# Kernel tuning notes

Hardware: AMD Instinct MI355X
Metric: run time of the kernel (lower is better)

## Reference

```python
import jax, jax.numpy as jnp
import numpy as np

N = 10000   # nodes
E = 320000  # edges
B = 4       # batch
D = 128     # in_dim == out_dim
H = 4       # heads
DH = D // H # 32, per-head dim
OUT_L = D // H  # per-layer out_fc output dim (out_dim/num_heads)
NEG_SLOPE = 0.1


def setup_inputs() -> dict:
    key = jax.random.key(0)
    ks = jax.random.split(key, 20)
    inp = {
        "features": jax.random.normal(ks[0], (B, N, D), dtype=jnp.float32),
        "src": jax.random.randint(ks[1], (E,), 0, N),
        "dst": jax.random.randint(ks[2], (E,), 0, N),
        "edge_w": jax.random.uniform(ks[3], (E,), dtype=jnp.float32),
    }
    s = 0.05
    for l in range(2):
        k = 4 + 5 * l
        inp[f"fc_w{l}"] = jax.random.normal(ks[k], (D, D), dtype=jnp.float32) * s
        inp[f"al{l}"] = jax.random.normal(ks[k + 1], (H, DH), dtype=jnp.float32) * s
        inp[f"ar{l}"] = jax.random.normal(ks[k + 2], (H, DH), dtype=jnp.float32) * s
        inp[f"out_w{l}"] = jax.random.normal(ks[k + 3], (OUT_L, DH), dtype=jnp.float32) * s
        inp[f"out_b{l}"] = jnp.zeros((OUT_L,), dtype=jnp.float32)
    inp["mlp_w"] = jax.random.normal(ks[14], (D, 2 * D), dtype=jnp.float32) * s
    inp["mlp_b"] = jnp.zeros((D,), dtype=jnp.float32)
    return inp


def _gat_layer(x, src, dst, w, fc_w, al, ar, out_w, out_b):
    # x: [B,N,D]
    feat = jnp.einsum("bnd,ed->bne", x, fc_w).reshape(B, N, H, DH)  # fc, no bias
    el = jnp.einsum("bnhd,hd->bnh", feat, al)  # [B,N,H]
    er = jnp.einsum("bnhd,hd->bnh", feat, ar)
    # per-edge scores, edge-major: [E,B,H]
    e = jnp.moveaxis(el[:, src] + er[:, dst], 1, 0)
    e = jnp.where(e > 0, e, NEG_SLOPE * e)        # LeakyReLU(0.1)
    e = e * w[:, None, None]                      # edge weight applied pre-softmax
    # edge-softmax over incoming edges of each dst node
    m = jax.ops.segment_max(e, dst, num_segments=N)
    m = jnp.where(jnp.isfinite(m), m, 0.0)
    ex = jnp.exp(e - m[dst])
    den = jax.ops.segment_sum(ex, dst, num_segments=N)[dst]
    a = ex / jnp.where(den == 0, 1.0, den)        # [E,B,H]
    # u_mul_e + sum aggregation
    feat_n = jnp.moveaxis(feat, 0, 1)             # [N,B,H,DH]
    msg = feat_n[src] * a[..., None]              # [E,B,H,DH]
    agg = jax.ops.segment_sum(msg, dst, num_segments=N)  # [N,B,H,DH]
    out = jax.nn.relu(jnp.einsum("nbhd,od->nbho", agg, out_w) + out_b)
    # transpose(0,1) then concat heads along feature dim -> [B,N,H*OUT_L]
    return jnp.moveaxis(out, 0, 1).reshape(B, N, H * OUT_L)


def reference(features, src, dst, edge_w,
              fc_w0, al0, ar0, out_w0, out_b0,
              fc_w1, al1, ar1, out_w1, out_b1,
              mlp_w, mlp_b):
    x1 = _gat_layer(features, src, dst, edge_w, fc_w0, al0, ar0, out_w0, out_b0)
    x2 = _gat_layer(x1, src, dst, edge_w, fc_w1, al1, ar1, out_w1, out_b1)
    h = jnp.concatenate([x1, x2], axis=-1)        # [B,N,2*D]
    return jnp.einsum("bnk,ok->bno", h, mlp_w) + mlp_b  # eval mode: dropout off
```

## Files before the change

kernel.cpp:

```cpp
#include <hip/hip_runtime.h>
#include <hip/hip_fp16.h>
#include <float.h>

#define NN 10000
#define EE 320000
#define BB 4
#define DD 128
#define HH 4
#define DHH 32

union H4 { uint2 u2; __half2 h2[2]; };
union H8 { float4 f4; __half2 h2[4]; };

typedef _Float16 f16x8 __attribute__((ext_vector_type(8)));
typedef float f32x4 __attribute__((ext_vector_type(4)));


__global__ void prep_kernel(const float* __restrict__ fc0, const float* __restrict__ fc1,
                            const float* __restrict__ mlp,
                            __half* __restrict__ bp0, __half* __restrict__ bp1,
                            __half* __restrict__ bpm,
                            const int* __restrict__ dst, int* __restrict__ cnt) {
    if (blockIdx.x < 128) {
        int s = blockIdx.x * 256 + threadIdx.x;
        int i = s & 7, l = (s >> 3) & 63, ct = (s >> 9) & 7, kt = s >> 12;
        int k = kt * 32 + 8 * (l >> 4) + i;
        int o = ct * 16 + (l & 15);
        bpm[s] = __float2half(mlp[o * 256 + k]);
        if (s < 16384) {
            bp0[s] = __float2half(fc0[o * 128 + k]);
            bp1[s] = __float2half(fc1[o * 128 + k]);
        }
    } else {
        int e = (blockIdx.x - 128) * 256 + threadIdx.x;
        if (e < EE) atomicAdd(&cnt[dst[e]], 1);
    }
}

__global__ void scan_kernel(const int* __restrict__ cnt, int* __restrict__ row_off) {
    __shared__ int part[16];
    int t = threadIdx.x;
    int lane = t & 63, wv = t >> 6;
    const int CH = 10;
    int loc[CH];
    int s = 0;
#pragma unroll
    for (int j = 0; j < CH; ++j) {
        int i = t * CH + j;
        int v = (i < NN) ? cnt[i] : 0;
        loc[j] = s;
        s += v;
    }
    int x = s;
#pragma unroll
    for (int off = 1; off < 64; off <<= 1) {
        int y = __shfl_up(x, off, 64);
        if (lane >= off) x += y;
    }
    if (lane == 63) part[wv] = x;
    __syncthreads();
    if (t == 0) {
        int a = 0;
#pragma unroll
        for (int w = 0; w < 16; ++w) { int v = part[w]; part[w] = a; a += v; }
    }
    __syncthreads();
    int base = part[wv] + (x - s);
#pragma unroll
    for (int j = 0; j < CH; ++j) {
        int i = t * CH + j;
        if (i < NN) row_off[i] = base + loc[j];
    }
    if (t == 1023) row_off[NN] = base + s;
}

template <int K, int REMAP, bool A_HALF, bool ATTN, bool HALF_OUT, bool BIAS>
__device__ __forceinline__ void gemm_body(
    __half* A_s, const void* A_, int lda,
    const __half* __restrict__ Bp,
    const float* al, const float* ar, const float* bias,
    __half* outh, float* outf, int ldo,
    float* el_out, float* er_out, int block) {
    int tid = threadIdx.x;
    int row0 = block * 64;

    if (A_HALF) {
        const __half* A = (const __half*)A_;
#pragma unroll
        for (int it = 0; it < (64 * K / 8) / 256; ++it) {
            int s = it * 256 + tid;
            int r = s / (K / 8), c8 = s % (K / 8);
            uint4 v = *reinterpret_cast<const uint4*>(A + (size_t)(row0 + r) * lda + c8 * 8);
            int byte = (r * K + c8 * 8) * 2;
            byte ^= (r & 7) << 4;
            *reinterpret_cast<uint4*>((char*)A_s + byte) = v;
        }
    } else {
        const float* A = (const float*)A_;
#pragma unroll
        for (int it = 0; it < (64 * K / 4) / 256; ++it) {
            int s = it * 256 + tid;
            int r = s / (K / 4), c4 = s % (K / 4);
            float4 v = *reinterpret_cast<const float4*>(A + (size_t)(row0 + r) * lda + c4 * 4);
            __half h[4];
            h[0] = __float2half(v.x); h[1] = __float2half(v.y);
            h[2] = __float2half(v.z); h[3] = __float2half(v.w);
            int byte = (r * K + c4 * 4) * 2;
            byte ^= (r & 7) << 4;
            *reinterpret_cast<uint2*>((char*)A_s + byte) = *reinterpret_cast<uint2*>(h);
        }
    }
    __syncthreads();

    int l = tid & 63, w = tid >> 6;
    int g = l >> 4, r15 = l & 15;
    f32x4 acc[8] = {};

#pragma unroll
    for (int kt = 0; kt < K / 32; ++kt) {
        int row = w * 16 + r15;
        int byte = (row * K + kt * 32 + 8 * g) * 2;
        byte ^= (row & 7) << 4;
        f16x8 a = *reinterpret_cast<const f16x8*>((const char*)A_s + byte);
        const f16x8* bp = reinterpret_cast<const f16x8*>(Bp) + (size_t)(kt * 8) * 64 + l;
#pragma unroll
        for (int ct = 0; ct < 8; ++ct) {
            f16x8 b = bp[(size_t)ct * 64];
            acc[ct] = __builtin_amdgcn_mfma_f32_16x16x32_f16(a, b, acc[ct], 0, 0, 0);
        }
    }

    int grow[4];
#pragma unroll
    for (int reg = 0; reg < 4; ++reg) {
        int r = row0 + w * 16 + g * 4 + reg;
        if (REMAP == 0) grow[reg] = r;
        else if (REMAP == 1) { int n = r % NN, b = r / NN; grow[reg] = n * 4 + b; }
        else grow[reg] = (r & 3) * NN + (r >> 2);
    }
#pragma unroll
    for (int ct = 0; ct < 8; ++ct) {
        int col = ct * 16 + r15;
#pragma unroll
        for (int reg = 0; reg < 4; ++reg) {
            float v = acc[ct][reg];
            if (BIAS) v += bias[col];
            if (HALF_OUT) outh[(size_t)grow[reg] * ldo + col] = __float2half(v);
            else outf[(size_t)grow[reg] * ldo + col] = v;
        }
    }

    if (ATTN) {
#pragma unroll
        for (int h = 0; h < 4; ++h) {
            float a0 = al[(2 * h) * 16 + r15], a1 = al[(2 * h + 1) * 16 + r15];
            float b0 = ar[(2 * h) * 16 + r15], b1 = ar[(2 * h + 1) * 16 + r15];
            f32x4 pe, pr;
#pragma unroll
            for (int reg = 0; reg < 4; ++reg) {
                pe[reg] = acc[2 * h][reg] * a0 + acc[2 * h + 1][reg] * a1;
                pr[reg] = acc[2 * h][reg] * b0 + acc[2 * h + 1][reg] * b1;
            }
#pragma unroll
            for (int mk = 1; mk <= 8; mk <<= 1) {
#pragma unroll
                for (int reg = 0; reg < 4; ++reg) {
                    pe[reg] += __shfl_xor(pe[reg], mk, 64);
                    pr[reg] += __shfl_xor(pr[reg], mk, 64);
                }
            }
            if (r15 == 0) {
#pragma unroll
                for (int reg = 0; reg < 4; ++reg) {
                    el_out[grow[reg] * 4 + h] = pe[reg];
                    er_out[grow[reg] * 4 + h] = pr[reg];
                }
            }
        }
    }
}

template <int K, int REMAP, bool A_HALF, bool ATTN, bool HALF_OUT, bool BIAS>
__global__ __launch_bounds__(256) void mfma_gemm(
    const void* __restrict__ A_, int lda,
    const __half* __restrict__ Bp,
    const float* __restrict__ al, const float* __restrict__ ar,
    const float* __restrict__ bias,
    __half* __restrict__ outh, float* __restrict__ outf, int ldo,
    float* __restrict__ el_out, float* __restrict__ er_out) {
    __shared__ __half A_s[64 * K];
    gemm_body<K, REMAP, A_HALF, ATTN, HALF_OUT, BIAS>(
        A_s, A_, lda, Bp, al, ar, bias, outh, outf, ldo, el_out, er_out, blockIdx.x);
}

__global__ __launch_bounds__(256) void gemm0_scatter(
    const float* __restrict__ A, const __half* __restrict__ bp0,
    const float* __restrict__ al0, const float* __restrict__ ar0,
    __half* __restrict__ feat_h, float* __restrict__ el, float* __restrict__ er,
    const int* __restrict__ dst, const int* __restrict__ row_off,
    int* __restrict__ cursor, int* __restrict__ edge_ids) {
    __shared__ __half A_s[64 * 128];
    if (blockIdx.x >= 625) {
        int e = (blockIdx.x - 625) * 256 + threadIdx.x;
        if (e < EE) {
            int d = dst[e];
            int p = atomicAdd(&cursor[d], 1);
            edge_ids[row_off[d] + p] = e;
        }
        return;
    }
    gemm_body<128, 1, false, true, true, false>(
        A_s, A, 128, bp0, al0, ar0, nullptr, feat_h, nullptr, 128, el, er, blockIdx.x);
}

__global__ __launch_bounds__(256) void gat_aggregate(
    const int* __restrict__ row_off, const int* __restrict__ edge_ids,
    const int* __restrict__ src, const float* __restrict__ ew,
    const float* __restrict__ el, const float* __restrict__ er,
    const __half* __restrict__ feat_h, const float* __restrict__ out_w,
    const float* __restrict__ out_b, __half* __restrict__ hcat, int layer_off) {
    __shared__ float s_owt[32 * 33];
    __shared__ int s_srcA[4][64];
    __shared__ float s_wA[4][64];
    __shared__ float s_aggA[4][16 * 33];

    int tid = threadIdx.x;
    for (int i = tid; i < 1024; i += 256) {
        int o = i >> 5, d = i & 31;
        s_owt[d * 33 + o] = out_w[i];
    }
    __syncthreads();

    int wv = tid >> 6, lane = tid & 63;
    int n = blockIdx.x * 4 + wv;
    int start = row_off[n], end = row_off[n + 1];
    int* s_src = s_srcA[wv];
    float* s_w = s_wA[wv];
    float* s_agg = s_aggA[wv];

    int bh4 = lane >> 2, sl = lane & 3;
    float er1 = er[(size_t)n * 16 + bh4];
    const float* el_base = el + bh4;
    const __half* fbase = feat_h + lane * 8;

    float den = 0.f;
    float acc8[8];
#pragma unroll
    for (int i = 0; i < 8; ++i) acc8[i] = 0.f;

    for (int base = start; base < end; base += 64) {
        int cnum = end - base;
        if (cnum > 64) cnum = 64;
        if (lane < cnum) {
            int eid = edge_ids[base + lane];
            s_src[lane] = src[eid];
            s_w[lane] = ew[eid];
        }
#pragma unroll 8
        for (int j = 0; j < cnum; ++j) {
            int s = s_src[j];
            float sc = el_base[(size_t)s * 16] + er1;
            sc = sc > 0.f ? sc : 0.1f * sc;
            sc *= s_w[j];
            float p = __expf(sc);
            den += p;
            H8 u;
            u.f4 = *reinterpret_cast<const float4*>(fbase + (size_t)s * 512);
            float2 f0 = __half22float2(u.h2[0]);
            float2 f1 = __half22float2(u.h2[1]);
            float2 f2 = __half22float2(u.h2[2]);
            float2 f3 = __half22float2(u.h2[3]);
            acc8[0] += p * f0.x; acc8[1] += p * f0.y;
            acc8[2] += p * f1.x; acc8[3] += p * f1.y;
            acc8[4] += p * f2.x; acc8[5] += p * f2.y;
            acc8[6] += p * f3.x; acc8[7] += p * f3.y;
        }
    }

    float inv_den = (den == 0.f) ? 1.f : 1.f / den;
#pragma unroll
    for (int i = 0; i < 8; ++i) s_agg[bh4 * 33 + sl * 8 + i] = acc8[i] * inv_den;

    float o_acc[8];
#pragma unroll
    for (int i = 0; i < 8; ++i) o_acc[i] = out_b[sl * 8 + i];
#pragma unroll 8
    for (int dd = 0; dd < 32; ++dd) {
        float a = s_agg[bh4 * 33 + dd];
        const float* wr = s_owt + dd * 33 + sl * 8;
#pragma unroll
        for (int i = 0; i < 8; ++i) o_acc[i] += a * wr[i];
    }
    H8 ov;
#pragma unroll
    for (int k = 0; k < 4; ++k)
        ov.h2[k] = __floats2half2_rn(fmaxf(o_acc[2 * k], 0.f), fmaxf(o_acc[2 * k + 1], 0.f));
    int b = bh4 >> 2, h = bh4 & 3;
    *reinterpret_cast<float4*>(hcat + ((size_t)(n * 4 + b)) * 256 + layer_off + h * 32 + sl * 8) = ov.f4;
}

extern "C" void kernel_launch(void* const* d_in, const int* in_sizes, int n_in,
                              void* d_out, int out_size, void* d_ws, size_t ws_size,
                              hipStream_t stream) {
    const float* features = (const float*)d_in[0];
    const int* src = (const int*)d_in[1];
    const int* dst = (const int*)d_in[2];
    const float* edge_w = (const float*)d_in[3];
    const float* fc_w0 = (const float*)d_in[4];
    const float* al0 = (const float*)d_in[5];
    const float* ar0 = (const float*)d_in[6];
    const float* out_w0 = (const float*)d_in[7];
    const float* out_b0 = (const float*)d_in[8];
    const float* fc_w1 = (const float*)d_in[9];
    const float* al1 = (const float*)d_in[10];
    const float* ar1 = (const float*)d_in[11];
    const float* out_w1 = (const float*)d_in[12];
    const float* out_b1 = (const float*)d_in[13];
    const float* mlp_w = (const float*)d_in[14];
    const float* mlp_b = (const float*)d_in[15];
    float* out = (float*)d_out;

    char* p = (char*)d_ws;
    auto take = [&](size_t bytes) {
        char* cur = p;
        p += (bytes + 255) & ~(size_t)255;
        return cur;
    };
    __half* bp0 = (__half*)take(16384 * 2);
    __half* bp1 = (__half*)take(16384 * 2);
    __half* bpm = (__half*)take(32768 * 2);
    __half* feat_h = (__half*)take((size_t)BB * NN * 128 * 2);
    __half* hcat = (__half*)take((size_t)BB * NN * 256 * 2);
    float* el = (float*)take((size_t)BB * NN * HH * 4);
    float* er = (float*)take((size_t)BB * NN * HH * 4);
    int* cnt = (int*)take((size_t)NN * 4);
    int* cursor = (int*)take((size_t)NN * 4);
    int* row_off = (int*)take((size_t)(NN + 1) * 4);
    int* edge_ids = (int*)take((size_t)EE * 4);
    (void)ws_size; (void)in_sizes; (void)n_in; (void)out_size;

    size_t zbytes = (size_t)((char*)cursor - (char*)cnt) + (size_t)NN * 4;
    hipMemsetAsync(cnt, 0, zbytes, stream);

    prep_kernel<<<128 + EE / 256, 256, 0, stream>>>(fc_w0, fc_w1, mlp_w, bp0, bp1, bpm, dst, cnt);
    scan_kernel<<<1, 1024, 0, stream>>>(cnt, row_off);

    const int GEMM_GRID = (BB * NN) / 64;
    const int AGG_GRID = NN / 4;

    gemm0_scatter<<<GEMM_GRID + EE / 256, 256, 0, stream>>>(
        features, bp0, al0, ar0, feat_h, el, er, dst, row_off, cursor, edge_ids);
    gat_aggregate<<<AGG_GRID, 256, 0, stream>>>(row_off, edge_ids, src, edge_w, el, er,
                                                feat_h, out_w0, out_b0, hcat, 0);
    mfma_gemm<128, 0, true, true, true, false><<<GEMM_GRID, 256, 0, stream>>>(
        hcat, 256, bp1, al1, ar1, nullptr, feat_h, nullptr, 128, el, er);
    gat_aggregate<<<AGG_GRID, 256, 0, stream>>>(row_off, edge_ids, src, edge_w, el, er,
                                                feat_h, out_w1, out_b1, hcat, 128);
    mfma_gemm<256, 2, true, false, false, true><<<GEMM_GRID, 256, 0, stream>>>(
        hcat, 256, bpm, nullptr, nullptr, mlp_b, nullptr, out, 128, nullptr, nullptr);
}
```

Measured before the change: 196.3 us.

## Split final MLP GEMM by K and fuse first half into layer-1 GEMM launch

The final MLP GEMM (K=256) is split into two K=128 halves. The half that uses x1 runs as extra blocks in the same launch as the layer-1 feature GEMM. The half that uses x2 runs after the second aggregation and accumulates into the output with read-modify-write. This moves half of the MLP work off the critical tail and shrinks the last kernel, at the cost of an extra read of the output. Correctness depends on the bpm offset of 16384 matching the packed weight layout for the second K half.

New measurement: 195.1 us. About the same (-0.6%).

```diff
diff --git a/kernel.cpp b/kernel.cpp
--- a/kernel.cpp
+++ b/kernel.cpp
@@ -74,7 +74,7 @@
     if (t == 1023) row_off[NN] = base + s;
 }
 
-template <int K, int REMAP, bool A_HALF, bool ATTN, bool HALF_OUT, bool BIAS>
+template <int K, int REMAP, bool A_HALF, bool ATTN, bool HALF_OUT, bool BIAS, bool ACCUM>
 __device__ __forceinline__ void gemm_body(
     __half* A_s, const void* A_, int lda,
     const __half* __restrict__ Bp,
@@ -146,6 +146,7 @@
             float v = acc[ct][reg];
             if (BIAS) v += bias[col];
             if (HALF_OUT) outh[(size_t)grow[reg] * ldo + col] = __float2half(v);
+            else if (ACCUM) outf[(size_t)grow[reg] * ldo + col] += v;
             else outf[(size_t)grow[reg] * ldo + col] = v;
         }
     }
@@ -180,7 +181,7 @@
     }
 }
 
-template <int K, int REMAP, bool A_HALF, bool ATTN, bool HALF_OUT, bool BIAS>
+template <int K, int REMAP, bool A_HALF, bool ATTN, bool HALF_OUT, bool BIAS, bool ACCUM>
 __global__ __launch_bounds__(256) void mfma_gemm(
     const void* __restrict__ A_, int lda,
     const __half* __restrict__ Bp,
@@ -189,7 +190,7 @@
     __half* __restrict__ outh, float* __restrict__ outf, int ldo,
     float* __restrict__ el_out, float* __restrict__ er_out) {
     __shared__ __half A_s[64 * K];
-    gemm_body<K, REMAP, A_HALF, ATTN, HALF_OUT, BIAS>(
+    gemm_body<K, REMAP, A_HALF, ATTN, HALF_OUT, BIAS, ACCUM>(
         A_s, A_, lda, Bp, al, ar, bias, outh, outf, ldo, el_out, er_out, blockIdx.x);
 }
 
@@ -209,8 +210,26 @@
         }
         return;
     }
-    gemm_body<128, 1, false, true, true, false>(
+    gemm_body<128, 1, false, true, true, false, false>(
         A_s, A, 128, bp0, al0, ar0, nullptr, feat_h, nullptr, 128, el, er, blockIdx.x);
+}
+
+__global__ __launch_bounds__(256) void gemm1_mlp1(
+    const __half* __restrict__ hcat, const __half* __restrict__ bp1,
+    const __half* __restrict__ bpm,
+    const float* __restrict__ al1, const float* __restrict__ ar1,
+    const float* __restrict__ mlp_b,
+    __half* __restrict__ feat_h, float* __restrict__ el, float* __restrict__ er,
+    float* __restrict__ out) {
+    __shared__ __half A_s[64 * 128];
+    if (blockIdx.x < 625) {
+        gemm_body<128, 0, true, true, true, false, false>(
+            A_s, hcat, 256, bp1, al1, ar1, nullptr, feat_h, nullptr, 128, el, er, blockIdx.x);
+    } else {
+        gemm_body<128, 2, true, false, false, true, false>(
+            A_s, hcat, 256, bpm, nullptr, nullptr, mlp_b, nullptr, out, 128,
+            nullptr, nullptr, blockIdx.x - 625);
+    }
 }
 
 __global__ __launch_bounds__(256) void gat_aggregate(
@@ -352,10 +371,11 @@
         features, bp0, al0, ar0, feat_h, el, er, dst, row_off, cursor, edge_ids);
     gat_aggregate<<<AGG_GRID, 256, 0, stream>>>(row_off, edge_ids, src, edge_w, el, er,
                                                 feat_h, out_w0, out_b0, hcat, 0);
-    mfma_gemm<128, 0, true, true, true, false><<<GEMM_GRID, 256, 0, stream>>>(
-        hcat, 256, bp1, al1, ar1, nullptr, feat_h, nullptr, 128, el, er);
+    gemm1_mlp1<<<2 * GEMM_GRID, 256, 0, stream>>>(
+        hcat, bp1, bpm, al1, ar1, mlp_b, feat_h, el, er, out);
     gat_aggregate<<<AGG_GRID, 256, 0, stream>>>(row_off, edge_ids, src, edge_w, el, er,
                                                 feat_h, out_w1, out_b1, hcat, 128);
-    mfma_gemm<256, 2, true, false, false, true><<<GEMM_GRID, 256, 0, stream>>>(
-        hcat, 256, bpm, nullptr, nullptr, mlp_b, nullptr, out, 128, nullptr, nullptr);
-}
+    mfma_gemm<128, 2, true, false, false, false, true><<<GEMM_GRID, 256, 0, stream>>>(
+        hcat + 128, 256, bpm + 16384, nullptr, nullptr, nullptr,
+        nullptr, out, 128, nullptr, nullptr);
+}
```
